# Performance work log

Hardware: AMD Instinct MI355X
Metric: run time of the kernel (lower is better)

The kernel has to match this reference:

```python
import jax, jax.numpy as jnp
import numpy as np

N_NODES = 100000
N_EDGES = 1600000
IN = 128
OUT = 32
HEADS = 4
NEG_SLOPE = 0.2


def setup_inputs() -> dict:
    key = jax.random.key(0)
    ks = jax.random.split(key, 6)
    x = jax.random.normal(ks[0], (N_NODES, IN), dtype=jnp.float32)
    row = jax.random.randint(ks[1], (N_EDGES,), 0, N_NODES, dtype=jnp.int32)
    col = jax.random.randint(ks[2], (N_EDGES,), 0, N_NODES, dtype=jnp.int32)
    W = jax.random.normal(ks[3], (OUT * HEADS, IN), dtype=jnp.float32) * (1.0 / np.sqrt(IN))
    b = jnp.zeros((OUT * HEADS,), dtype=jnp.float32)
    a_l = jax.random.normal(ks[4], (1, OUT, HEADS), dtype=jnp.float32) * 0.1
    a_r = jax.random.normal(ks[5], (1, OUT, HEADS), dtype=jnp.float32) * 0.1
    return {"x": x, "row": row, "col": col, "W": W, "b": b, "a_l": a_l, "a_r": a_r}


def reference(x, row, col, W, b, a_l, a_r):
    N = x.shape[0]
    # Z: [N, OUT, HEADS] (row-major view of [N, OUT*HEADS], matching torch .view)
    Z = (x @ W.T + b).reshape(N, OUT, HEADS)
    e_l = jnp.sum(Z * a_l, axis=1)  # [N, HEADS]
    e_r = jnp.sum(Z * a_r, axis=1)  # [N, HEADS]
    e = e_l[row] + e_r[col]         # [E, HEADS]
    e = jnp.where(e > 0, e, NEG_SLOPE * e)  # LeakyReLU
    # segment softmax over edges grouped by destination (row)
    m = jax.ops.segment_max(e, row, num_segments=N)      # [N, HEADS]
    ex = jnp.exp(e - m[row])                              # [E, HEADS]
    denom = jax.ops.segment_sum(ex, row, num_segments=N)  # [N, HEADS]
    alpha = ex / denom[row]                               # [E, HEADS]
    # bspmm: out[i,:,h] = sum_{(i,j) in E} alpha[e,h] * Z[j,:,h]
    out = jax.ops.segment_sum(alpha[:, None, :] * Z[col], row, num_segments=N)
    return out
```

## Files before the change

kernel.cpp:

```cpp
#include <hip/hip_runtime.h>
#include <hip/hip_bf16.h>
#include <math.h>


typedef __attribute__((ext_vector_type(8))) short bf16x8;
typedef __attribute__((ext_vector_type(4))) float f32x4;

__device__ __forceinline__ ushort f2bf(float f) {
  __hip_bfloat16 h = __float2bfloat16(f);
  return __builtin_bit_cast(ushort, h);
}
__device__ __forceinline__ float bf2f(ushort u) {
  unsigned v = ((unsigned)u) << 16;
  return __builtin_bit_cast(float, v);
}

__global__ __launch_bounds__(512) void prep0(
    const float* __restrict__ W, ushort* __restrict__ Wh,
    ushort* __restrict__ Wl, int* __restrict__ cntP, int N8) {
  int i = blockIdx.x * 512 + threadIdx.x;
  if (i < 16384) {
    float w = W[i];
    ushort hb = f2bf(w);
    Wh[i] = hb;
    Wl[i] = f2bf(w - bf2f(hb));
  }
  if (i < N8) cntP[i] = 0;
}

__global__ __launch_bounds__(512, 4) void gemm_z(
    const float* __restrict__ x, const ushort* __restrict__ Wh,
    const ushort* __restrict__ Wl, const float* __restrict__ bias,
    const float* __restrict__ a_l, const float* __restrict__ a_r,
    ushort* __restrict__ Zh, float* __restrict__ el, float* __restrict__ er,
    int N) {
  __shared__ __align__(16) ushort smem[16896];
  __shared__ float sal[128], sar[128];

  const int t = threadIdx.x;
  const int lane = t & 63;
  const int wv = t >> 6;
  const int row0 = blockIdx.x * 128;
  const int l15 = lane & 15, l4 = lane >> 4;
  const int ch = wv * 16 + l15;

  if (t < 128) { sal[t] = a_l[t]; sar[t] = a_r[t]; }

  bf16x8 Bh[4], Bl[4];
#pragma unroll
  for (int kf = 0; kf < 4; ++kf) {
    int off = ch * 128 + kf * 32 + l4 * 8;
    Bh[kf] = *(const bf16x8*)&Wh[off];
    Bl[kf] = *(const bf16x8*)&Wl[off];
  }

  ushort* xh = smem;
#pragma unroll
  for (int i = 0; i < 8; ++i) {
    int f4 = i * 512 + t;
    int r = f4 >> 5;
    int k = (f4 & 31) * 4;
    int gr = row0 + r;
    float4 v = make_float4(0.f, 0.f, 0.f, 0.f);
    if (gr < N) v = ((const float4*)x)[(size_t)gr * 32 + (f4 & 31)];
    int idx = r * 128 + (k ^ ((r & 7) << 3));
    uint2 hv;
    hv.x = f2bf(v.x) | ((unsigned)f2bf(v.y) << 16);
    hv.y = f2bf(v.z) | ((unsigned)f2bf(v.w) << 16);
    *(uint2*)&xh[idx] = hv;
  }
  __syncthreads();

  f32x4 acc[8];
#pragma unroll
  for (int rt = 0; rt < 8; ++rt) acc[rt] = (f32x4){0.f, 0.f, 0.f, 0.f};

#pragma unroll
  for (int kf = 0; kf < 4; ++kf) {
#pragma unroll
    for (int rt = 0; rt < 8; ++rt) {
      int r = rt * 16 + l15;
      int idx = r * 128 + ((kf * 32 + l4 * 8) ^ ((r & 7) << 3));
      bf16x8 ah = *(const bf16x8*)&xh[idx];
      acc[rt] = __builtin_amdgcn_mfma_f32_16x16x32_bf16(ah, Bh[kf], acc[rt], 0, 0, 0);
      acc[rt] = __builtin_amdgcn_mfma_f32_16x16x32_bf16(ah, Bl[kf], acc[rt], 0, 0, 0);
    }
  }
  __syncthreads();

  ushort* zs = smem;
  {
    float bv = bias[ch];
    int o = ch >> 2, h = ch & 3;
    int s = (o & 15) * 8 + h * 2 + (o >> 4);
#pragma unroll
    for (int rt = 0; rt < 8; ++rt) {
#pragma unroll
      for (int j = 0; j < 4; ++j) {
        int r = rt * 16 + l4 * 4 + j;
        zs[r * 132 + s] = f2bf(acc[rt][j] + bv);
      }
    }
  }
  __syncthreads();

  {
    int r = t >> 2;
    int h = t & 3;
    int gr = row0 + r;
    if (gr < N) {
#pragma unroll
      for (int q = 0; q < 4; ++q) {
        uint4 v = *(const uint4*)&zs[r * 132 + h * 32 + q * 8];
        *(uint4*)&Zh[(size_t)gr * 128 + h * 32 + q * 8] = v;
      }
      float sl = 0.f, sr = 0.f;
#pragma unroll
      for (int op = 0; op < 16; ++op) {
        unsigned zz = *(const unsigned*)&zs[r * 132 + op * 8 + h * 2];
        float zlo = bf2f((ushort)(zz & 0xffff));
        float zhi = bf2f((ushort)(zz >> 16));
        int c = (op << 2) + h;
        sl += zlo * sal[c] + zhi * sal[c + 64];
        sr += zlo * sar[c] + zhi * sar[c + 64];
      }
      el[(unsigned)gr * 4 + h] = sl;
      er[(unsigned)gr * 4 + h] = sr;
    }
  }
}

__global__ __launch_bounds__(256) void deg_rank(
    const int* __restrict__ row, int* __restrict__ cntP,
    int* __restrict__ rank, int E, int N) {
  int e = blockIdx.x * 256 + threadIdx.x;
  if (e >= E) return;
  int copy = blockIdx.x & 7;
  rank[e] = atomicAdd(&cntP[copy * N + row[e]], 1);
}

__global__ __launch_bounds__(256) void nscan(
    int* __restrict__ cntP, int* __restrict__ deg, int* __restrict__ base,
    int* __restrict__ bsum, int N) {
  __shared__ int ss[256];
  int t = threadIdx.x;
  int i = blockIdx.x * 256 + t;
  int tot = 0;
  if (i < N) {
    int run = 0;
#pragma unroll
    for (int k = 0; k < 8; ++k) {
      int c = cntP[k * N + i];
      cntP[k * N + i] = run;
      run += c;
    }
    tot = run;
  }
  ss[t] = tot;
  __syncthreads();
#pragma unroll
  for (int off = 1; off < 256; off <<= 1) {
    int u = (t >= off) ? ss[t - off] : 0;
    __syncthreads();
    ss[t] += u;
    __syncthreads();
  }
  if (i < N) {
    base[i] = ss[t] - tot;
    deg[i] = tot;
  }
  if (t == 255) bsum[blockIdx.x] = ss[255];
}

__global__ __launch_bounds__(512) void scan2(int* __restrict__ bsum, int NB) {
  __shared__ int s[512];
  int v = (threadIdx.x < NB) ? bsum[threadIdx.x] : 0;
  s[threadIdx.x] = v;
  __syncthreads();
#pragma unroll
  for (int off = 1; off < 512; off <<= 1) {
    int t = (threadIdx.x >= off) ? s[threadIdx.x - off] : 0;
    __syncthreads();
    s[threadIdx.x] += t;
    __syncthreads();
  }
  if (threadIdx.x < NB) bsum[threadIdx.x] = s[threadIdx.x] - v;
}

__global__ __launch_bounds__(256) void fill(
    const int* __restrict__ row, const int* __restrict__ col,
    const int* __restrict__ rank, const int* __restrict__ base,
    const int* __restrict__ bsum, const int* __restrict__ cntP,
    int* __restrict__ sorted_col, int E, int N) {
  int e = blockIdx.x * 256 + threadIdx.x;
  if (e >= E) return;
  int r = row[e];
  int copy = (e >> 8) & 7;
  int pos = base[r] + bsum[r >> 8] + cntP[copy * N + r] + rank[e];
  sorted_col[pos] = col[e];
}

__global__ __launch_bounds__(256) void gather(
    const int* __restrict__ base, const int* __restrict__ bsum,
    const int* __restrict__ deg, const int* __restrict__ sorted_col,
    const float* __restrict__ el, const float* __restrict__ er,
    const ushort* __restrict__ Zh, float* __restrict__ out, int N) {
  int t = threadIdx.x;
  int lane = t & 63;
  int n = blockIdx.x * 4 + (t >> 6);
  if (n >= N) return;
  int h = lane & 3;
  int jj = lane >> 2;
  int s = base[n] + bsum[n >> 8];
  int d = deg[n];
  int end = s + d;
  float elv = el[((unsigned)n << 2) + h];
  float acc0 = 0.f, acc1 = 0.f, sumA = 0.f;
  const unsigned* Zh32 = (const unsigned*)Zh;
  const unsigned zlane = (unsigned)lane;
  const int bpb = (lane & 3) << 2;

  for (int p = s; p < end; p += 16) {
    int vn = end - p;
    int cl6 = 0;
    float xv = 0.f;
    if (jj < vn) {
      int cl = sorted_col[p + jj];
      float e = elv + er[((unsigned)cl << 2) + h];
      e = fmaxf(e, 0.2f * e);
      xv = __expf(e);
      cl6 = cl << 6;
    }
    sumA += xv;
    float xvb[16];
    unsigned addr[16];
#pragma unroll
    for (int q = 0; q < 16; ++q) {
      int a = bpb + (q << 4);
      xvb[q] = __builtin_bit_cast(float,
          __builtin_amdgcn_ds_bpermute(a, __builtin_bit_cast(int, xv)));
      addr[q] = (unsigned)__builtin_amdgcn_ds_bpermute(a, cl6) + zlane;
    }
    unsigned zz[16];
#pragma unroll
    for (int q = 0; q < 16; ++q) zz[q] = Zh32[addr[q]];
#pragma unroll
    for (int q = 0; q < 16; ++q) {
      acc0 = fmaf(xvb[q], __builtin_bit_cast(float, zz[q] << 16), acc0);
      acc1 = fmaf(xvb[q], __builtin_bit_cast(float, zz[q] & 0xffff0000u), acc1);
    }
  }
  float sum = sumA;
  sum += __shfl_xor(sum, 4, 64);
  sum += __shfl_xor(sum, 8, 64);
  sum += __shfl_xor(sum, 16, 64);
  sum += __shfl_xor(sum, 32, 64);
  float inv = (d > 0) ? 1.0f / sum : 0.f;
  unsigned ob = ((unsigned)n << 7) + zlane;
  __builtin_nontemporal_store(acc0 * inv, &out[ob]);
  __builtin_nontemporal_store(acc1 * inv, &out[ob + 64]);
}

extern "C" void kernel_launch(void* const* d_in, const int* in_sizes, int n_in,
                              void* d_out, int out_size, void* d_ws, size_t ws_size,
                              hipStream_t stream) {
  const float* x   = (const float*)d_in[0];
  const int*   row = (const int*)d_in[1];
  const int*   col = (const int*)d_in[2];
  const float* W   = (const float*)d_in[3];
  const float* b   = (const float*)d_in[4];
  const float* a_l = (const float*)d_in[5];
  const float* a_r = (const float*)d_in[6];
  float* out = (float*)d_out;

  const int N = in_sizes[0] / 128;
  const int E = in_sizes[1];
  const int NB = (N + 255) / 256;

  char* w = (char*)d_ws;
  ushort* Zh       = (ushort*)w;             w += (size_t)N * 128 * 2;
  int*   sorted_col= (int*)w;                w += (size_t)E * 4;
  int*   rank      = (int*)w;                w += (size_t)E * 4;
  float* el        = (float*)w;              w += (size_t)N * 4 * 4;
  float* er        = (float*)w;              w += (size_t)N * 4 * 4;
  int*   cntP      = (int*)w;                w += (size_t)N * 8 * 4;
  int*   deg       = (int*)w;                w += (size_t)N * 4;
  int*   base      = (int*)w;                w += (size_t)N * 4;
  int*   bsum      = (int*)w;                w += 512 * 4;
  ushort* Wh       = (ushort*)w;             w += 16384 * 2;
  ushort* Wl       = (ushort*)w;             w += 16384 * 2;

  const int N8 = N * 8;
  const int P0 = (N8 > 16384 ? N8 : 16384);
  prep0<<<(P0 + 511) / 512, 512, 0, stream>>>(W, Wh, Wl, cntP, N8);

  gemm_z<<<(N + 127) / 128, 512, 0, stream>>>(x, Wh, Wl, b, a_l, a_r,
                                              Zh, el, er, N);
  deg_rank<<<(E + 255) / 256, 256, 0, stream>>>(row, cntP, rank, E, N);
  nscan<<<NB, 256, 0, stream>>>(cntP, deg, base, bsum, N);
  scan2<<<1, 512, 0, stream>>>(bsum, NB);
  fill<<<(E + 255) / 256, 256, 0, stream>>>(row, col, rank, base, bsum, cntP,
                                            sorted_col, E, N);
  gather<<<(N + 3) / 4, 256, 0, stream>>>(base, bsum, deg, sorted_col, el, er,
                                          Zh, out, N);
}
```

Before: 209.7 us.

## Fuse degree counting into GEMM launch and pack col/weight into one bpermute

```diff
diff --git a/kernel.cpp b/kernel.cpp
--- a/kernel.cpp
+++ b/kernel.cpp
@@ -28,14 +28,24 @@
   if (i < N8) cntP[i] = 0;
 }
 
-__global__ __launch_bounds__(512, 4) void gemm_z(
+__global__ __launch_bounds__(512, 4) void gemm_deg(
     const float* __restrict__ x, const ushort* __restrict__ Wh,
     const ushort* __restrict__ Wl, const float* __restrict__ bias,
     const float* __restrict__ a_l, const float* __restrict__ a_r,
     ushort* __restrict__ Zh, float* __restrict__ el, float* __restrict__ er,
-    int N) {
+    int N, const int* __restrict__ row, int* __restrict__ cntP,
+    int* __restrict__ rank, int E, int G1) {
   __shared__ __align__(16) ushort smem[16896];
   __shared__ float sal[128], sar[128];
+
+  if ((int)blockIdx.x >= G1) {
+    int e = ((int)blockIdx.x - G1) * 512 + threadIdx.x;
+    if (e < E) {
+      int copy = blockIdx.x & 7;
+      rank[e] = atomicAdd(&cntP[copy * N + row[e]], 1);
+    }
+    return;
+  }
 
   const int t = threadIdx.x;
   const int lane = t & 63;
@@ -130,15 +140,6 @@
   }
 }
 
-__global__ __launch_bounds__(256) void deg_rank(
-    const int* __restrict__ row, int* __restrict__ cntP,
-    int* __restrict__ rank, int E, int N) {
-  int e = blockIdx.x * 256 + threadIdx.x;
-  if (e >= E) return;
-  int copy = blockIdx.x & 7;
-  rank[e] = atomicAdd(&cntP[copy * N + row[e]], 1);
-}
-
 __global__ __launch_bounds__(256) void nscan(
     int* __restrict__ cntP, int* __restrict__ deg, int* __restrict__ base,
     int* __restrict__ bsum, int N) {
@@ -191,11 +192,11 @@
     const int* __restrict__ row, const int* __restrict__ col,
     const int* __restrict__ rank, const int* __restrict__ base,
     const int* __restrict__ bsum, const int* __restrict__ cntP,
-    int* __restrict__ sorted_col, int E, int N) {
+    int* __restrict__ sorted_col, int E, int N, int G1) {
   int e = blockIdx.x * 256 + threadIdx.x;
   if (e >= E) return;
   int r = row[e];
-  int copy = (e >> 8) & 7;
+  int copy = (G1 + (e >> 9)) & 7;
   int pos = base[r] + bsum[r >> 8] + cntP[copy * N + r] + rank[e];
   sorted_col[pos] = col[e];
 }
@@ -222,28 +223,28 @@
 
   for (int p = s; p < end; p += 16) {
     int vn = end - p;
-    int cl6 = 0;
+    unsigned pk = 0;
     float xv = 0.f;
     if (jj < vn) {
       int cl = sorted_col[p + jj];
       float e = elv + er[((unsigned)cl << 2) + h];
       e = fmaxf(e, 0.2f * e);
       xv = __expf(e);
-      cl6 = cl << 6;
+      pk = ((unsigned)cl << 15) | (f2bf(xv) & 0x7fffu);
     }
     sumA += xv;
     float xvb[16];
-    unsigned addr[16];
+    unsigned addrv[16];
 #pragma unroll
     for (int q = 0; q < 16; ++q) {
       int a = bpb + (q << 4);
-      xvb[q] = __builtin_bit_cast(float,
-          __builtin_amdgcn_ds_bpermute(a, __builtin_bit_cast(int, xv)));
-      addr[q] = (unsigned)__builtin_amdgcn_ds_bpermute(a, cl6) + zlane;
+      unsigned b = (unsigned)__builtin_amdgcn_ds_bpermute(a, (int)pk);
+      addrv[q] = ((b >> 15) << 6) + zlane;
+      xvb[q] = bf2f((ushort)(b & 0x7fffu));
     }
     unsigned zz[16];
 #pragma unroll
-    for (int q = 0; q < 16; ++q) zz[q] = Zh32[addr[q]];
+    for (int q = 0; q < 16; ++q) zz[q] = Zh32[addrv[q]];
 #pragma unroll
     for (int q = 0; q < 16; ++q) {
       acc0 = fmaf(xvb[q], __builtin_bit_cast(float, zz[q] << 16), acc0);
@@ -294,13 +295,15 @@
   const int P0 = (N8 > 16384 ? N8 : 16384);
   prep0<<<(P0 + 511) / 512, 512, 0, stream>>>(W, Wh, Wl, cntP, N8);
 
-  gemm_z<<<(N + 127) / 128, 512, 0, stream>>>(x, Wh, Wl, b, a_l, a_r,
-                                              Zh, el, er, N);
-  deg_rank<<<(E + 255) / 256, 256, 0, stream>>>(row, cntP, rank, E, N);
+  const int G1 = (N + 127) / 128;
+  const int G2 = (E + 511) / 512;
+  gemm_deg<<<G1 + G2, 512, 0, stream>>>(x, Wh, Wl, b, a_l, a_r, Zh, el, er,
+                                        N, row, cntP, rank, E, G1);
+
   nscan<<<NB, 256, 0, stream>>>(cntP, deg, base, bsum, N);
   scan2<<<1, 512, 0, stream>>>(bsum, NB);
   fill<<<(E + 255) / 256, 256, 0, stream>>>(row, col, rank, base, bsum, cntP,
-                                            sorted_col, E, N);
+                                            sorted_col, E, N, G1);
   gather<<<(N + 3) / 4, 256, 0, stream>>>(base, bsum, deg, sorted_col, el, er,
                                           Zh, out, N);
 }
```

New measurement: 201.5 us. -3.9%, faster.
